# Optimization experiments

Hardware: AMD Instinct MI355X
Metric: run time of the kernel (lower is better)

The kernel has to match this reference:

```python
import jax, jax.numpy as jnp
import numpy as np

K = 7            # kernel size per spatial dim
HALF = K // 2    # 3
WIN = K * K      # 49


def _rel_dist():
    # matches torch: meshgrid('ij') of arange(k)-k//2, euclidean dist, flattened row-major
    c = np.arange(K, dtype=np.float32) - HALF
    gi, gj = np.meshgrid(c, c, indexing='ij')
    return jnp.asarray(np.sqrt(gi ** 2 + gj ** 2).reshape(-1))


def _unfold2d(t):
    B, H, W, C = t.shape
    p = jnp.pad(t, ((0, 0), (HALF, HALF), (HALF, HALF), (0, 0)))
    wins = [p[:, i:i + H, j:j + W, :] for i in range(K) for j in range(K)]
    return jnp.stack(wins, axis=3)


def setup_inputs() -> dict:
    key = jax.random.key(0)
    k1, k2, k3, k4, k5 = jax.random.split(key, 5)
    B, H, W, C = 4, 64, 64, 128
    x = jax.random.normal(k1, (B, H, W, C), dtype=jnp.float32)
    W_qkv = jax.random.normal(k2, (C, 3 * C), dtype=jnp.float32) * (C ** -0.5)
    # width_proj is zero-initialized in the module; use small random values to exercise the soft mask
    W_width = jax.random.normal(k3, (C, 1), dtype=jnp.float32) * 0.02
    b_width = jax.random.normal(k4, (1,), dtype=jnp.float32) * 0.02
    W_out = jax.random.normal(k5, (C, C), dtype=jnp.float32) * (C ** -0.5)
    return {"x": x, "W_qkv": W_qkv, "W_width": W_width, "b_width": b_width, "W_out": W_out}


def reference(x, W_qkv, W_width, b_width, W_out):
    B, H, W, C = x.shape
    L = H * W
    scale = C ** -0.5
    rel_dist = _rel_dist()
    max_dist = rel_dist.max()

    qkv = x @ W_qkv                              # (B,H,W,3C)
    q, k, v = jnp.split(qkv, 3, axis=-1)
    width = jax.nn.sigmoid(x @ W_width + b_width) * max_dist + 0.5  # (B,H,W,1)

    k_win = _unfold2d(k).reshape(B, L, WIN, C)
    v_win = _unfold2d(v).reshape(B, L, WIN, C)
    q_flat = q.reshape(B, L, C)
    width_flat = width.reshape(B, L, 1)

    scores = jnp.einsum('blc,blwc->blw', q_flat, k_win) * scale
    soft_mask = jax.nn.sigmoid((width_flat - rel_dist) * 5.0)
    scores = scores - (1.0 - soft_mask) * 10000.0
    attn = jax.nn.softmax(scores, axis=-1)
    out = jnp.einsum('blw,blwc->blc', attn, v_win).reshape(B, H, W, C)
    return (out + v) @ W_out
```

## Files before the change

### kernel.cpp

```cpp
#include <hip/hip_runtime.h>

#define C 128
#define NPIX 16384
#define THREE_C 384

typedef unsigned short u16;
typedef unsigned int u32;
typedef short bf16x8 __attribute__((ext_vector_type(8)));
typedef float f32x4 __attribute__((ext_vector_type(4)));

__device__ __forceinline__ float bf2f(u16 h) { return __uint_as_float(((u32)h) << 16); }
__device__ __forceinline__ u16 f2bf(float f) {
    u32 b = __float_as_uint(f);
    b += 0x7FFF + ((b >> 16) & 1);
    return (u16)(b >> 16);
}
__device__ __forceinline__ u32 pack2(float a, float b) {
    return (u32)f2bf(a) | ((u32)f2bf(b) << 16);
}

#define GST 136

__global__ __launch_bounds__(256) void qkv_kernel(const float* __restrict__ x,
                                                  const float* __restrict__ Wqkv,
                                                  const float* __restrict__ Wwidth,
                                                  const float* __restrict__ bwidth,
                                                  const float* __restrict__ Wout,
                                                  u16* __restrict__ qb,
                                                  u16* __restrict__ kb,
                                                  u16* __restrict__ vb,
                                                  float* __restrict__ width_g,
                                                  u16* __restrict__ wot) {
    __shared__ u16 xs[64 * GST];
    __shared__ u16 wt[128 * GST];
    const int task = ((int)(blockIdx.x & 7)) * 96 + ((int)blockIdx.x >> 3);
    const int rb = task / 3;
    const int nb = task % 3;
    const int p0 = rb * 64;
    const int tid = threadIdx.x;
    const int wv = tid >> 6;
    const int l = tid & 63;
    const int l15 = l & 15;
    const int l4 = l >> 4;

#pragma unroll
    for (int t = 0; t < 8; ++t) {
        const int f = tid + t * 256;
        const int kq = f & 31, r = f >> 5;
        const float4 xv = *(const float4*)(x + (size_t)(p0 + r) * C + kq * 4);
        uint2 pk;
        pk.x = pack2(xv.x, xv.y);
        pk.y = pack2(xv.z, xv.w);
        *(uint2*)&xs[r * GST + kq * 4] = pk;
    }
#pragma unroll
    for (int t = 0; t < 16; ++t) {
        const int f = tid + t * 256;
        const int c = f & 127, kq = f >> 7;
        const float w0 = Wqkv[(size_t)(kq * 4 + 0) * THREE_C + nb * 128 + c];
        const float w1 = Wqkv[(size_t)(kq * 4 + 1) * THREE_C + nb * 128 + c];
        const float w2 = Wqkv[(size_t)(kq * 4 + 2) * THREE_C + nb * 128 + c];
        const float w3 = Wqkv[(size_t)(kq * 4 + 3) * THREE_C + nb * 128 + c];
        uint2 pk;
        pk.x = pack2(w0, w1);
        pk.y = pack2(w2, w3);
        *(uint2*)&wt[c * GST + kq * 4] = pk;
    }
    if (task < 8) {
        const int base = (task * 256 + tid) * 8;
        const int c = base >> 7, k0 = base & 127;
        uint4 pk;
        pk.x = pack2(Wout[(size_t)(k0 + 0) * C + c], Wout[(size_t)(k0 + 1) * C + c]);
        pk.y = pack2(Wout[(size_t)(k0 + 2) * C + c], Wout[(size_t)(k0 + 3) * C + c]);
        pk.z = pack2(Wout[(size_t)(k0 + 4) * C + c], Wout[(size_t)(k0 + 5) * C + c]);
        pk.w = pack2(Wout[(size_t)(k0 + 6) * C + c], Wout[(size_t)(k0 + 7) * C + c]);
        *(uint4*)&wot[base] = pk;
    }
    __syncthreads();

    if (nb == 0 && tid < 64) {
        float wacc = 0.f;
#pragma unroll
        for (int kk = 0; kk < C; ++kk) wacc += bf2f(xs[tid * GST + kk]) * Wwidth[kk];
        const float z = wacc + bwidth[0];
        width_g[p0 + tid] = (1.f / (1.f + __expf(-z))) * 4.242640687f + 0.5f;
    }

    const int strip = wv * 16;
    bf16x8 af[4];
#pragma unroll
    for (int kf = 0; kf < 4; ++kf)
        af[kf] = *(const bf16x8*)&xs[(strip + l15) * GST + kf * 32 + l4 * 8];

    f32x4 acc[8];
#pragma unroll
    for (int nf = 0; nf < 8; ++nf) acc[nf] = (f32x4){0.f, 0.f, 0.f, 0.f};
#pragma unroll
    for (int nf = 0; nf < 8; ++nf) {
#pragma unroll
        for (int kf = 0; kf < 4; ++kf) {
            const bf16x8 bf = *(const bf16x8*)&wt[(nf * 16 + l15) * GST + kf * 32 + l4 * 8];
            acc[nf] = __builtin_amdgcn_mfma_f32_16x16x32_bf16(af[kf], bf, acc[nf], 0, 0, 0);
        }
    }

    u16* dst = (nb == 0) ? qb : (nb == 1) ? kb : vb;
#pragma unroll
    for (int nf = 0; nf < 8; ++nf) {
        const int col = nf * 16 + l15;
#pragma unroll
        for (int r = 0; r < 4; ++r) {
            const int row = strip + l4 * 4 + r;
            dst[(size_t)(p0 + row) * C + col] = f2bf(acc[nf][r]);
        }
    }
}

#define HSTRIDE 136
#define TSTRIDE 236
#define VSWZ(ch, h) ((h) ^ ((((ch) >> 3) & 3) << 3))

__global__ __launch_bounds__(1024) void attn_kernel(const u16* __restrict__ qb,
                                                    const u16* __restrict__ kb,
                                                    const u16* __restrict__ vb,
                                                    const float* __restrict__ width_g,
                                                    const u16* __restrict__ wot,
                                                    float* __restrict__ out) {
    __shared__ u16 Kl[208 * HSTRIDE];
    __shared__ u16 Vt[128 * TSTRIDE];
    __shared__ u16 Pl[64 * TSTRIDE];
    __shared__ float rsum[4][64];
    __shared__ float wdl[64];

    const int tid = threadIdx.x;
    const int wv = tid >> 6;
    const int l = tid & 63;
    const int l15 = l & 15;
    const int l4 = l >> 4;

    const int W = ((int)blockIdx.x & 7) * 32 + ((int)blockIdx.x >> 3);
    const int b = W >> 6;
    const int t = W & 63;
    const int i0 = (t >> 3) * 8;
    const int j0 = (t & 7) * 8;
    const int pbase = b * 4096;

    if (tid < 64)
        wdl[tid] = width_g[pbase + (i0 + (tid >> 3)) * 64 + j0 + (tid & 7)];

    const uint4 z4 = make_uint4(0, 0, 0, 0);
    uint4 kreg[4];
    int koff[4];
    bool kw[4];
#pragma unroll
    for (int rr = 0; rr < 4; ++rr) {
        const int f = tid + rr * 1024;
        kw[rr] = (f < 3328);
        kreg[rr] = z4;
        const int c = f & 15, h = f >> 4;
        koff[rr] = h * HSTRIDE + c * 8;
        if (kw[rr] && h < 196) {
            const int hi = (h * 2341) >> 15;
            const int hj = h - hi * 14;
            const int ii = i0 - 3 + hi, jj = j0 - 3 + hj;
            if (((unsigned)ii < 64u) && ((unsigned)jj < 64u))
                kreg[rr] = *(const uint4*)(kb + (size_t)(pbase + ii * 64 + jj) * C + c * 8);
        }
    }
    uint4 va[2], vz[2];
    int vc8[2], vh[2];
    bool vw[2];
#pragma unroll
    for (int rr = 0; rr < 2; ++rr) {
        const int f = tid + rr * 1024;
        vw[rr] = (f < 1792);
        va[rr] = z4; vz[rr] = z4;
        const int c8 = f & 15, h = ((f >> 4) * 2) & 255;
        vc8[rr] = c8; vh[rr] = h;
        if (vw[rr]) {
            {
                const int hi = (h * 2341) >> 15;
                const int hj = h - hi * 14;
                const int ii = i0 - 3 + hi, jj = j0 - 3 + hj;
                if ((h < 196) && ((unsigned)ii < 64u) && ((unsigned)jj < 64u))
                    va[rr] = *(const uint4*)(vb + (size_t)(pbase + ii * 64 + jj) * C + c8 * 8);
            }
            {
                const int h1 = h + 1;
                const int hi = (h1 * 2341) >> 15;
                const int hj = h1 - hi * 14;
                const int ii = i0 - 3 + hi, jj = j0 - 3 + hj;
                if ((h1 < 196) && ((unsigned)ii < 64u) && ((unsigned)jj < 64u))
                    vz[rr] = *(const uint4*)(vb + (size_t)(pbase + ii * 64 + jj) * C + c8 * 8);
            }
        }
    }
#pragma unroll
    for (int rr = 0; rr < 4; ++rr)
        if (kw[rr]) *(uint4*)&Kl[koff[rr]] = kreg[rr];
#pragma unroll
    for (int rr = 0; rr < 2; ++rr) {
        if (vw[rr]) {
            union { uint4 u4; u16 us[8]; } ua, uz;
            ua.u4 = va[rr]; uz.u4 = vz[rr];
            const int c8 = vc8[rr], h = vh[rr];
#pragma unroll
            for (int s = 0; s < 8; ++s) {
                const int ch = c8 * 8 + s;
                *(u32*)&Vt[ch * TSTRIDE + VSWZ(ch, h)] = (u32)ua.us[s] | ((u32)uz.us[s] << 16);
            }
        }
    }

    const int strip = wv >> 2;
    const int g = wv & 3;
    bf16x8 qf[4];
    {
        const int qr = strip * 16 + l15;
        const int p = pbase + (i0 + (qr >> 3)) * 64 + j0 + (qr & 7);
#pragma unroll
        for (int kf = 0; kf < 4; ++kf)
            qf[kf] = *(const bf16x8*)(qb + (size_t)p * C + kf * 32 + l4 * 8);
    }
    __syncthreads();

    f32x4 sv[4];
#pragma unroll
    for (int tt = 0; tt < 4; ++tt) {
        const int nf = g + 4 * tt;
        f32x4 acc = {0.f, 0.f, 0.f, 0.f};
        if (nf < 13) {
            const u16* kr = Kl + (nf * 16 + l15) * HSTRIDE + l4 * 8;
#pragma unroll
            for (int kf = 0; kf < 4; ++kf)
                acc = __builtin_amdgcn_mfma_f32_16x16x32_bf16(
                    qf[kf], *(const bf16x8*)(kr + kf * 32), acc, 0, 0, 0);
        }
        sv[tt] = acc;
    }

    uint4 wcopy0 = *(const uint4*)(wot + tid * 8);
    uint4 wcopy1 = *(const uint4*)(wot + (tid + 1024) * 8);

    const int qrb = strip * 16 + l4 * 4;
    float wdr[4];
#pragma unroll
    for (int r = 0; r < 4; ++r) wdr[r] = wdl[qrb + r];
    float smr[4] = {0.f, 0.f, 0.f, 0.f};
#pragma unroll
    for (int tt = 0; tt < 4; ++tt) {
        const int nf = g + 4 * tt;
        if (nf < 13) {
            const int n = nf * 16 + l15;
            const int hi = (n * 2341) >> 15;
            const int hj = n - hi * 14;
#pragma unroll
            for (int r = 0; r < 4; ++r) {
                const int qr = qrb + r;
                const int di = hi - 3 - (qr >> 3);
                const int dj = hj - 3 - (qr & 7);
                const bool valid = ((unsigned)(di + 3) <= 6u) && ((unsigned)(dj + 3) <= 6u);
                float e = 0.f;
                if (valid) {
                    const float rd = sqrtf((float)(di * di + dj * dj));
                    const float sm = 1.f / (1.f + __expf(-5.f * (wdr[r] - rd)));
                    e = __expf(sv[tt][r] * 0.08838834765f - (1.f - sm) * 10000.f);
                }
                sv[tt][r] = e;
                smr[r] += e;
                Pl[qr * TSTRIDE + n] = f2bf(e);
            }
        } else if (nf == 13) {
            const int n = 208 + l15;
#pragma unroll
            for (int r = 0; r < 4; ++r)
                Pl[(qrb + r) * TSTRIDE + n] = 0;
        }
    }
#pragma unroll
    for (int r = 0; r < 4; ++r) {
        float s = smr[r];
        s += __shfl_xor(s, 1);
        s += __shfl_xor(s, 2);
        s += __shfl_xor(s, 4);
        s += __shfl_xor(s, 8);
        smr[r] = s;
    }
    if (l15 == 0) {
#pragma unroll
        for (int r = 0; r < 4; ++r) rsum[g][qrb + r] = smr[r];
    }
    __syncthreads();

    u16* wtl = Kl;
    {
        const int c0 = tid >> 4, k0 = (tid & 15) * 8;
        *(uint4*)&wtl[c0 * GST + k0] = wcopy0;
        const int c1 = 64 + (tid >> 4);
        *(uint4*)&wtl[c1 * GST + k0] = wcopy1;
    }

    float invr[4];
#pragma unroll
    for (int r = 0; r < 4; ++r) {
        const int qr = qrb + r;
        invr[r] = 1.f / (rsum[0][qr] + rsum[1][qr] + rsum[2][qr] + rsum[3][qr]);
    }

    f32x4 oacc[2];
    oacc[0] = (f32x4){0.f, 0.f, 0.f, 0.f};
    oacc[1] = (f32x4){0.f, 0.f, 0.f, 0.f};
#pragma unroll
    for (int kf = 0; kf < 7; ++kf) {
        const bf16x8 pa = *(const bf16x8*)(Pl + (strip * 16 + l15) * TSTRIDE + kf * 32 + l4 * 8);
#pragma unroll
        for (int nf2 = 0; nf2 < 2; ++nf2) {
            const int ch = g * 32 + nf2 * 16 + l15;
            const bf16x8 vf = *(const bf16x8*)(Vt + ch * TSTRIDE + VSWZ(ch, kf * 32 + l4 * 8));
            oacc[nf2] = __builtin_amdgcn_mfma_f32_16x16x32_bf16(pa, vf, oacc[nf2], 0, 0, 0);
        }
    }

    u16* ylds = Kl + 128 * GST;
#pragma unroll
    for (int nf2 = 0; nf2 < 2; ++nf2) {
        const int cch = g * 32 + nf2 * 16 + l15;
#pragma unroll
        for (int r = 0; r < 4; ++r) {
            const int qr = qrb + r;
            const int h = 45 + (qr >> 3) * 14 + (qr & 7);
            const float vv = bf2f(Vt[cch * TSTRIDE + VSWZ(cch, h)]);
            ylds[qr * GST + cch] = f2bf(oacc[nf2][r] * invr[r] + vv);
        }
    }
    __syncthreads();

    bf16x8 yf[4];
#pragma unroll
    for (int kf = 0; kf < 4; ++kf)
        yf[kf] = *(const bf16x8*)&ylds[(strip * 16 + l15) * GST + kf * 32 + l4 * 8];

    f32x4 oc[2];
    oc[0] = (f32x4){0.f, 0.f, 0.f, 0.f};
    oc[1] = (f32x4){0.f, 0.f, 0.f, 0.f};
#pragma unroll
    for (int u = 0; u < 2; ++u) {
        const int nf = g + 4 * u;
#pragma unroll
        for (int kf = 0; kf < 4; ++kf) {
            const bf16x8 bf = *(const bf16x8*)&wtl[(nf * 16 + l15) * GST + kf * 32 + l4 * 8];
            oc[u] = __builtin_amdgcn_mfma_f32_16x16x32_bf16(yf[kf], bf, oc[u], 0, 0, 0);
        }
    }
#pragma unroll
    for (int u = 0; u < 2; ++u) {
        const int col = (g + 4 * u) * 16 + l15;
#pragma unroll
        for (int r = 0; r < 4; ++r) {
            const int qr = qrb + r;
            const int p = pbase + (i0 + (qr >> 3)) * 64 + j0 + (qr & 7);
            out[(size_t)p * C + col] = oc[u][r];
        }
    }
}

extern "C" void kernel_launch(void* const* d_in, const int* in_sizes, int n_in,
                              void* d_out, int out_size, void* d_ws, size_t ws_size,
                              hipStream_t stream) {
    const float* x      = (const float*)d_in[0];
    const float* Wqkv   = (const float*)d_in[1];
    const float* Wwidth = (const float*)d_in[2];
    const float* bwidth = (const float*)d_in[3];
    const float* Wout   = (const float*)d_in[4];
    float* out = (float*)d_out;

    u16* qb = (u16*)d_ws;
    u16* kb = qb + (size_t)NPIX * C;
    u16* vb = kb + (size_t)NPIX * C;
    float* width = (float*)(vb + (size_t)NPIX * C);
    u16* wot = (u16*)(width + NPIX);

    qkv_kernel<<<768, 256, 0, stream>>>(x, Wqkv, Wwidth, bwidth, Wout, qb, kb, vb, width, wot);
    attn_kernel<<<256, 1024, 0, stream>>>(qb, kb, vb, width, wot, out);
}
```

Measured before the change: 26.96 us.

## Fold Q and K projections into a precomputed Wk·Wqᵀ matrix

Q and K are no longer materialized. Scores are computed as x_q · M · x_kᵀ with M = Wk·Wqᵀ, which a small side job in the prep kernel computes. The prep kernel now only computes V, width and a bf16 copy of x, which roughly thirds its GEMM work and global writes. The attention kernel loads x windows instead of K and does an extra small 64x128x128 MFMA per tile. It also needs extra LDS, more barriers and an extra bf16 rounding of the intermediate x·M product.

```diff
diff --git a/kernel.cpp b/kernel.cpp
--- a/kernel.cpp
+++ b/kernel.cpp
@@ -21,97 +21,161 @@
 
 #define GST 136
 
-__global__ __launch_bounds__(256) void qkv_kernel(const float* __restrict__ x,
-                                                  const float* __restrict__ Wqkv,
-                                                  const float* __restrict__ Wwidth,
-                                                  const float* __restrict__ bwidth,
-                                                  const float* __restrict__ Wout,
-                                                  u16* __restrict__ qb,
-                                                  u16* __restrict__ kb,
-                                                  u16* __restrict__ vb,
-                                                  float* __restrict__ width_g,
-                                                  u16* __restrict__ wot) {
-    __shared__ u16 xs[64 * GST];
-    __shared__ u16 wt[128 * GST];
-    const int task = ((int)(blockIdx.x & 7)) * 96 + ((int)blockIdx.x >> 3);
-    const int rb = task / 3;
-    const int nb = task % 3;
-    const int p0 = rb * 64;
+__global__ __launch_bounds__(256) void vprep_kernel(const float* __restrict__ x,
+                                                    const float* __restrict__ Wqkv,
+                                                    const float* __restrict__ Wwidth,
+                                                    const float* __restrict__ bwidth,
+                                                    const float* __restrict__ Wout,
+                                                    u16* __restrict__ xbb,
+                                                    u16* __restrict__ vb,
+                                                    float* __restrict__ width_g,
+                                                    u16* __restrict__ wot,
+                                                    u16* __restrict__ mtw) {
+    __shared__ u16 SL[26112];
+    const int bid = blockIdx.x;
     const int tid = threadIdx.x;
     const int wv = tid >> 6;
     const int l = tid & 63;
     const int l15 = l & 15;
     const int l4 = l >> 4;
 
-#pragma unroll
-    for (int t = 0; t < 8; ++t) {
-        const int f = tid + t * 256;
-        const int kq = f & 31, r = f >> 5;
-        const float4 xv = *(const float4*)(x + (size_t)(p0 + r) * C + kq * 4);
-        uint2 pk;
-        pk.x = pack2(xv.x, xv.y);
-        pk.y = pack2(xv.z, xv.w);
-        *(uint2*)&xs[r * GST + kq * 4] = pk;
-    }
-#pragma unroll
-    for (int t = 0; t < 16; ++t) {
-        const int f = tid + t * 256;
-        const int c = f & 127, kq = f >> 7;
-        const float w0 = Wqkv[(size_t)(kq * 4 + 0) * THREE_C + nb * 128 + c];
-        const float w1 = Wqkv[(size_t)(kq * 4 + 1) * THREE_C + nb * 128 + c];
-        const float w2 = Wqkv[(size_t)(kq * 4 + 2) * THREE_C + nb * 128 + c];
-        const float w3 = Wqkv[(size_t)(kq * 4 + 3) * THREE_C + nb * 128 + c];
-        uint2 pk;
-        pk.x = pack2(w0, w1);
-        pk.y = pack2(w2, w3);
-        *(uint2*)&wt[c * GST + kq * 4] = pk;
-    }
-    if (task < 8) {
-        const int base = (task * 256 + tid) * 8;
-        const int c = base >> 7, k0 = base & 127;
-        uint4 pk;
-        pk.x = pack2(Wout[(size_t)(k0 + 0) * C + c], Wout[(size_t)(k0 + 1) * C + c]);
-        pk.y = pack2(Wout[(size_t)(k0 + 2) * C + c], Wout[(size_t)(k0 + 3) * C + c]);
-        pk.z = pack2(Wout[(size_t)(k0 + 4) * C + c], Wout[(size_t)(k0 + 5) * C + c]);
-        pk.w = pack2(Wout[(size_t)(k0 + 6) * C + c], Wout[(size_t)(k0 + 7) * C + c]);
-        *(uint4*)&wot[base] = pk;
-    }
-    __syncthreads();
-
-    if (nb == 0 && tid < 64) {
-        float wacc = 0.f;
-#pragma unroll
-        for (int kk = 0; kk < C; ++kk) wacc += bf2f(xs[tid * GST + kk]) * Wwidth[kk];
-        const float z = wacc + bwidth[0];
-        width_g[p0 + tid] = (1.f / (1.f + __expf(-z))) * 4.242640687f + 0.5f;
-    }
-
-    const int strip = wv * 16;
-    bf16x8 af[4];
-#pragma unroll
-    for (int kf = 0; kf < 4; ++kf)
-        af[kf] = *(const bf16x8*)&xs[(strip + l15) * GST + kf * 32 + l4 * 8];
-
-    f32x4 acc[8];
-#pragma unroll
-    for (int nf = 0; nf < 8; ++nf) acc[nf] = (f32x4){0.f, 0.f, 0.f, 0.f};
-#pragma unroll
-    for (int nf = 0; nf < 8; ++nf) {
-#pragma unroll
-        for (int kf = 0; kf < 4; ++kf) {
-            const bf16x8 bf = *(const bf16x8*)&wt[(nf * 16 + l15) * GST + kf * 32 + l4 * 8];
-            acc[nf] = __builtin_amdgcn_mfma_f32_16x16x32_bf16(af[kf], bf, acc[nf], 0, 0, 0);
-        }
-    }
-
-    u16* dst = (nb == 0) ? qb : (nb == 1) ? kb : vb;
-#pragma unroll
-    for (int nf = 0; nf < 8; ++nf) {
-        const int col = nf * 16 + l15;
-#pragma unroll
-        for (int r = 0; r < 4; ++r) {
-            const int row = strip + l4 * 4 + r;
-            dst[(size_t)(p0 + row) * C + col] = f2bf(acc[nf][r]);
+    if (bid < 512) {
+        u16* xs = SL;
+        u16* wt = SL + 32 * GST;
+        const int task = ((bid & 7) << 6) + (bid >> 3);
+        const int p0 = task * 32;
+
+#pragma unroll
+        for (int t = 0; t < 4; ++t) {
+            const int f = tid + t * 256;
+            const int kq = f & 31, r = f >> 5;
+            const float4 xv = *(const float4*)(x + (size_t)(p0 + r) * C + kq * 4);
+            uint2 pk;
+            pk.x = pack2(xv.x, xv.y);
+            pk.y = pack2(xv.z, xv.w);
+            *(uint2*)&xs[r * GST + kq * 4] = pk;
+        }
+#pragma unroll
+        for (int t = 0; t < 16; ++t) {
+            const int f = tid + t * 256;
+            const int c = f & 127, kq = f >> 7;
+            const float w0 = Wqkv[(size_t)(kq * 4 + 0) * THREE_C + 256 + c];
+            const float w1 = Wqkv[(size_t)(kq * 4 + 1) * THREE_C + 256 + c];
+            const float w2 = Wqkv[(size_t)(kq * 4 + 2) * THREE_C + 256 + c];
+            const float w3 = Wqkv[(size_t)(kq * 4 + 3) * THREE_C + 256 + c];
+            uint2 pk;
+            pk.x = pack2(w0, w1);
+            pk.y = pack2(w2, w3);
+            *(uint2*)&wt[c * GST + kq * 4] = pk;
+        }
+        __syncthreads();
+
+        if (tid < 32) {
+            float wacc = 0.f;
+#pragma unroll
+            for (int kk = 0; kk < C; ++kk) wacc += bf2f(xs[tid * GST + kk]) * Wwidth[kk];
+            const float z = wacc + bwidth[0];
+            width_g[p0 + tid] = (1.f / (1.f + __expf(-z))) * 4.242640687f + 0.5f;
+        }
+
+#pragma unroll
+        for (int i = 0; i < 2; ++i) {
+            const int id = tid + 256 * i;
+            const int r = id >> 4, c16 = id & 15;
+            *(uint4*)(xbb + (size_t)(p0 + r) * C + c16 * 8) = *(const uint4*)&xs[r * GST + c16 * 8];
+        }
+
+        const int strip = (wv & 1) * 16;
+        const int nh = wv >> 1;
+        bf16x8 af[4];
+#pragma unroll
+        for (int kf = 0; kf < 4; ++kf)
+            af[kf] = *(const bf16x8*)&xs[(strip + l15) * GST + kf * 32 + l4 * 8];
+        f32x4 acc[4];
+#pragma unroll
+        for (int i = 0; i < 4; ++i) acc[i] = (f32x4){0.f, 0.f, 0.f, 0.f};
+#pragma unroll
+        for (int nfi = 0; nfi < 4; ++nfi) {
+            const int nf = nh * 4 + nfi;
+#pragma unroll
+            for (int kf = 0; kf < 4; ++kf) {
+                const bf16x8 bf = *(const bf16x8*)&wt[(nf * 16 + l15) * GST + kf * 32 + l4 * 8];
+                acc[nfi] = __builtin_amdgcn_mfma_f32_16x16x32_bf16(af[kf], bf, acc[nfi], 0, 0, 0);
+            }
+        }
+#pragma unroll
+        for (int nfi = 0; nfi < 4; ++nfi) {
+            const int col = (nh * 4 + nfi) * 16 + l15;
+#pragma unroll
+            for (int r = 0; r < 4; ++r) {
+                const int row = strip + l4 * 4 + r;
+                vb[(size_t)(p0 + row) * C + col] = f2bf(acc[nfi][r]);
+            }
+        }
+    } else {
+        u16* wkl = SL;
+        u16* wql = SL + 64 * GST;
+        const int blk = bid - 512;
+        const int d0 = blk * 64;
+
+#pragma unroll
+        for (int t = 0; t < 8; ++t) {
+            const int f = tid + t * 256;
+            const int kq = f & 31, r = f >> 5;
+            const float4 wv4 = *(const float4*)(Wqkv + (size_t)(d0 + r) * THREE_C + 128 + kq * 4);
+            uint2 pk;
+            pk.x = pack2(wv4.x, wv4.y);
+            pk.y = pack2(wv4.z, wv4.w);
+            *(uint2*)&wkl[r * GST + kq * 4] = pk;
+        }
+#pragma unroll
+        for (int t = 0; t < 16; ++t) {
+            const int f = tid + t * 256;
+            const int kq = f & 31, r = f >> 7 == 0 ? (f >> 5) : (f >> 5);
+            const int rr = f >> 5;
+            const float4 wv4 = *(const float4*)(Wqkv + (size_t)rr * THREE_C + kq * 4);
+            uint2 pk;
+            pk.x = pack2(wv4.x, wv4.y);
+            pk.y = pack2(wv4.z, wv4.w);
+            *(uint2*)&wql[rr * GST + kq * 4] = pk;
+        }
+#pragma unroll
+        for (int it = 0; it < 4; ++it) {
+            const int u4i = blk * 1024 + tid + 256 * it;
+            const int base = u4i * 8;
+            const int c = base >> 7, k0 = base & 127;
+            uint4 pk;
+            pk.x = pack2(Wout[(size_t)(k0 + 0) * C + c], Wout[(size_t)(k0 + 1) * C + c]);
+            pk.y = pack2(Wout[(size_t)(k0 + 2) * C + c], Wout[(size_t)(k0 + 3) * C + c]);
+            pk.z = pack2(Wout[(size_t)(k0 + 4) * C + c], Wout[(size_t)(k0 + 5) * C + c]);
+            pk.w = pack2(Wout[(size_t)(k0 + 6) * C + c], Wout[(size_t)(k0 + 7) * C + c]);
+            *(uint4*)&wot[base] = pk;
+        }
+        __syncthreads();
+
+        bf16x8 af[4];
+#pragma unroll
+        for (int kf = 0; kf < 4; ++kf)
+            af[kf] = *(const bf16x8*)&wkl[(wv * 16 + l15) * GST + kf * 32 + l4 * 8];
+        f32x4 acc[8];
+#pragma unroll
+        for (int nf = 0; nf < 8; ++nf) acc[nf] = (f32x4){0.f, 0.f, 0.f, 0.f};
+#pragma unroll
+        for (int nf = 0; nf < 8; ++nf) {
+#pragma unroll
+            for (int kf = 0; kf < 4; ++kf) {
+                const bf16x8 bf = *(const bf16x8*)&wql[(nf * 16 + l15) * GST + kf * 32 + l4 * 8];
+                acc[nf] = __builtin_amdgcn_mfma_f32_16x16x32_bf16(af[kf], bf, acc[nf], 0, 0, 0);
+            }
+        }
+#pragma unroll
+        for (int nf = 0; nf < 8; ++nf) {
+            const int c = nf * 16 + l15;
+#pragma unroll
+            for (int r = 0; r < 4; ++r) {
+                const int d = d0 + wv * 16 + l4 * 4 + r;
+                mtw[(size_t)d * C + c] = f2bf(acc[nf][r]);
+            }
         }
     }
 }
@@ -120,17 +184,18 @@
 #define TSTRIDE 236
 #define VSWZ(ch, h) ((h) ^ ((((ch) >> 3) & 3) << 3))
 
-__global__ __launch_bounds__(1024) void attn_kernel(const u16* __restrict__ qb,
-                                                    const u16* __restrict__ kb,
+__global__ __launch_bounds__(1024) void attn_kernel(const u16* __restrict__ xbb,
                                                     const u16* __restrict__ vb,
                                                     const float* __restrict__ width_g,
                                                     const u16* __restrict__ wot,
+                                                    const u16* __restrict__ mtw,
                                                     float* __restrict__ out) {
-    __shared__ u16 Kl[208 * HSTRIDE];
-    __shared__ u16 Vt[128 * TSTRIDE];
-    __shared__ u16 Pl[64 * TSTRIDE];
+    __shared__ u16 SL[75904];
     __shared__ float rsum[4][64];
     __shared__ float wdl[64];
+    u16* Xl = SL;
+    u16* MT = SL + 208 * HSTRIDE;
+    u16* Vt = MT + 128 * GST;
 
     const int tid = threadIdx.x;
     const int wv = tid >> 6;
@@ -164,7 +229,7 @@
             const int hj = h - hi * 14;
             const int ii = i0 - 3 + hi, jj = j0 - 3 + hj;
             if (((unsigned)ii < 64u) && ((unsigned)jj < 64u))
-                kreg[rr] = *(const uint4*)(kb + (size_t)(pbase + ii * 64 + jj) * C + c * 8);
+                kreg[rr] = *(const uint4*)(xbb + (size_t)(pbase + ii * 64 + jj) * C + c * 8);
         }
     }
     uint4 va[2], vz[2];
@@ -195,9 +260,18 @@
             }
         }
     }
+    uint4 mcp[2];
+    int moff[2];
+#pragma unroll
+    for (int i = 0; i < 2; ++i) {
+        const int id = tid + 1024 * i;
+        const int d = id >> 4, c8 = id & 15;
+        mcp[i] = *(const uint4*)(mtw + (size_t)d * C + c8 * 8);
+        moff[i] = d * GST + c8 * 8;
+    }
 #pragma unroll
     for (int rr = 0; rr < 4; ++rr)
-        if (kw[rr]) *(uint4*)&Kl[koff[rr]] = kreg[rr];
+        if (kw[rr]) *(uint4*)&Xl[koff[rr]] = kreg[rr];
 #pragma unroll
     for (int rr = 0; rr < 2; ++rr) {
         if (vw[rr]) {
@@ -211,30 +285,61 @@
             }
         }
     }
+#pragma unroll
+    for (int i = 0; i < 2; ++i) *(uint4*)&MT[moff[i]] = mcp[i];
+    __syncthreads();
 
     const int strip = wv >> 2;
     const int g = wv & 3;
-    bf16x8 qf[4];
+    bf16x8 xf[4];
     {
         const int qr = strip * 16 + l15;
-        const int p = pbase + (i0 + (qr >> 3)) * 64 + j0 + (qr & 7);
+        const int hown = 45 + (qr >> 3) * 14 + (qr & 7);
 #pragma unroll
         for (int kf = 0; kf < 4; ++kf)
-            qf[kf] = *(const bf16x8*)(qb + (size_t)p * C + kf * 32 + l4 * 8);
-    }
-    __syncthreads();
-
+            xf[kf] = *(const bf16x8*)&Xl[hown * HSTRIDE + kf * 32 + l4 * 8];
+    }
+    f32x4 tacc[2];
+    tacc[0] = (f32x4){0.f, 0.f, 0.f, 0.f};
+    tacc[1] = (f32x4){0.f, 0.f, 0.f, 0.f};
+#pragma unroll
+    for (int u = 0; u < 2; ++u) {
+        const int nf = g + 4 * u;
+#pragma unroll
+        for (int kf = 0; kf < 4; ++kf) {
+            const bf16x8 bf = *(const bf16x8*)&MT[(nf * 16 + l15) * GST + kf * 32 + l4 * 8];
+            tacc[u] = __builtin_amdgcn_mfma_f32_16x16x32_bf16(xf[kf], bf, tacc[u], 0, 0, 0);
+        }
+    }
+    __syncthreads();
+
+    u16* TD = MT;
+#pragma unroll
+    for (int u = 0; u < 2; ++u) {
+        const int col = (g + 4 * u) * 16 + l15;
+#pragma unroll
+        for (int r = 0; r < 4; ++r) {
+            const int row = strip * 16 + l4 * 4 + r;
+            TD[row * GST + col] = f2bf(tacc[u][r]);
+        }
+    }
+    __syncthreads();
+
+    bf16x8 tf[4];
+#pragma unroll
+    for (int kf = 0; kf < 4; ++kf)
+        tf[kf] = *(const bf16x8*)&TD[(strip * 16 + l15) * GST + kf * 32 + l4 * 8];
     f32x4 sv[4];
 #pragma unroll
     for (int tt = 0; tt < 4; ++tt) {
         const int nf = g + 4 * tt;
         f32x4 acc = {0.f, 0.f, 0.f, 0.f};
         if (nf < 13) {
-            const u16* kr = Kl + (nf * 16 + l15) * HSTRIDE + l4 * 8;
+            const u16* xr = Xl + (nf * 16 + l15) * HSTRIDE + l4 * 8;
 #pragma unroll
             for (int kf = 0; kf < 4; ++kf)
                 acc = __builtin_amdgcn_mfma_f32_16x16x32_bf16(
-                    qf[kf], *(const bf16x8*)(kr + kf * 32), acc, 0, 0, 0);
+                    tf[kf], *(const bf16x8*)(xr + kf * 32), acc, 0, 0, 0);
         }
         sv[tt] = acc;
     }
@@ -268,13 +373,7 @@
                 }
                 sv[tt][r] = e;
                 smr[r] += e;
-                Pl[qr * TSTRIDE + n] = f2bf(e);
-            }
-        } else if (nf == 13) {
-            const int n = 208 + l15;
-#pragma unroll
-            for (int r = 0; r < 4; ++r)
-                Pl[(qrb + r) * TSTRIDE + n] = 0;
+            }
         }
     }
 #pragma unroll
@@ -292,27 +391,43 @@
     }
     __syncthreads();
 
-    u16* wtl = Kl;
+    u16* Pb = Xl;
+    u16* YL = Xl + 64 * TSTRIDE;
+    u16* WO = MT;
+#pragma unroll
+    for (int tt = 0; tt < 4; ++tt) {
+        const int nf = g + 4 * tt;
+        if (nf < 13) {
+            const int n = nf * 16 + l15;
+#pragma unroll
+            for (int r = 0; r < 4; ++r)
+                Pb[(qrb + r) * TSTRIDE + n] = f2bf(sv[tt][r]);
+        } else if (nf == 13) {
+            const int n = 208 + l15;
+#pragma unroll
+            for (int r = 0; r < 4; ++r)
+                Pb[(qrb + r) * TSTRIDE + n] = 0;
+        }
+    }
     {
         const int c0 = tid >> 4, k0 = (tid & 15) * 8;
-        *(uint4*)&wtl[c0 * GST + k0] = wcopy0;
-        const int c1 = 64 + (tid >> 4);
-        *(uint4*)&wtl[c1 * GST + k0] = wcopy1;
-    }
-
+        *(uint4*)&WO[c0 * GST + k0] = wcopy0;
+        *(uint4*)&WO[(64 + c0) * GST + k0] = wcopy1;
+    }
     float invr[4];
 #pragma unroll
     for (int r = 0; r < 4; ++r) {
         const int qr = qrb + r;
         invr[r] = 1.f / (rsum[0][qr] + rsum[1][qr] + rsum[2][qr] + rsum[3][qr]);
     }
+    __syncthreads();
 
     f32x4 oacc[2];
     oacc[0] = (f32x4){0.f, 0.f, 0.f, 0.f};
     oacc[1] = (f32x4){0.f, 0.f, 0.f, 0.f};
 #pragma unroll
     for (int kf = 0; kf < 7; ++kf) {
-        const bf16x8 pa = *(const bf16x8*)(Pl + (strip * 16 + l15) * TSTRIDE + kf * 32 + l4 * 8);
+        const bf16x8 pa = *(const bf16x8*)(Pb + (strip * 16 + l15) * TSTRIDE + kf * 32 + l4 * 8);
 #pragma unroll
         for (int nf2 = 0; nf2 < 2; ++nf2) {
             const int ch = g * 32 + nf2 * 16 + l15;
@@ -320,8 +435,6 @@
             oacc[nf2] = __builtin_amdgcn_mfma_f32_16x16x32_bf16(pa, vf, oacc[nf2], 0, 0, 0);
         }
     }
-
-    u16* ylds = Kl + 128 * GST;
 #pragma unroll
     for (int nf2 = 0; nf2 < 2; ++nf2) {
         const int cch = g * 32 + nf2 * 16 + l15;
@@ -330,7 +443,7 @@
             const int qr = qrb + r;
             const int h = 45 + (qr >> 3) * 14 + (qr & 7);
             const float vv = bf2f(Vt[cch * TSTRIDE + VSWZ(cch, h)]);
-            ylds[qr * GST + cch] = f2bf(oacc[nf2][r] * invr[r] + vv);
+            YL[qr * GST + cch] = f2bf(oacc[nf2][r] * invr[r] + vv);
         }
     }
     __syncthreads();
@@ -338,8 +451,7 @@
     bf16x8 yf[4];
 #pragma unroll
     for (int kf = 0; kf < 4; ++kf)
-        yf[kf] = *(const bf16x8*)&ylds[(strip * 16 + l15) * GST + kf * 32 + l4 * 8];
-
+        yf[kf] = *(const bf16x8*)&YL[(strip * 16 + l15) * GST + kf * 32 + l4 * 8];
     f32x4 oc[2];
     oc[0] = (f32x4){0.f, 0.f, 0.f, 0.f};
     oc[1] = (f32x4){0.f, 0.f, 0.f, 0.f};
@@ -348,7 +460,7 @@
         const int nf = g + 4 * u;
 #pragma unroll
         for (int kf = 0; kf < 4; ++kf) {
-            const bf16x8 bf = *(const bf16x8*)&wtl[(nf * 16 + l15) * GST + kf * 32 + l4 * 8];
+            const bf16x8 bf = *(const bf16x8*)&WO[(nf * 16 + l15) * GST + kf * 32 + l4 * 8];
             oc[u] = __builtin_amdgcn_mfma_f32_16x16x32_bf16(yf[kf], bf, oc[u], 0, 0, 0);
         }
     }
@@ -374,12 +486,12 @@
     const float* Wout   = (const float*)d_in[4];
     float* out = (float*)d_out;
 
-    u16* qb = (u16*)d_ws;
-    u16* kb = qb + (size_t)NPIX * C;
-    u16* vb = kb + (size_t)NPIX * C;
+    u16* xbb = (u16*)d_ws;
+    u16* vb  = xbb + (size_t)NPIX * C;
     float* width = (float*)(vb + (size_t)NPIX * C);
     u16* wot = (u16*)(width + NPIX);
-
-    qkv_kernel<<<768, 256, 0, stream>>>(x, Wqkv, Wwidth, bwidth, Wout, qb, kb, vb, width, wot);
-    attn_kernel<<<256, 1024, 0, stream>>>(qb, kb, vb, width, wot, out);
+    u16* mtw = wot + 128 * 128;
+
+    vprep_kernel<<<514, 256, 0, stream>>>(x, Wqkv, Wwidth, bwidth, Wout, xbb, vb, width, wot, mtw);
+    attn_kernel<<<256, 1024, 0, stream>>>(xbb, vb, width, wot, mtw, out);
 }
```

New measurement: 36.86 us. +36.7%, slower.

## Shrink attention tile to 4x4 pixels with 1024 blocks of 512 threads

Applied to the files above, without the earlier changes.

The attention kernel now handles a 4x4 query tile with a 10x10 halo instead of an 8x8 tile with a 14x14 halo. It launches 1024 blocks of 512 threads with launch bounds allowing four blocks per CU, and loads W_out fragments straight from global memory into registers instead of staging them in LDS. The aim is more blocks and better occupancy on the 256-CU device, where 256 large blocks underfill it. The cost is more redundant K/V halo loading per output pixel (100 vs 196 halo rows for 16 vs 64 queries), and the V swizzle is dropped, so LDS bank conflicts may appear.

```diff
diff --git a/kernel.cpp b/kernel.cpp
--- a/kernel.cpp
+++ b/kernel.cpp
@@ -116,21 +116,19 @@
     }
 }
 
-#define HSTRIDE 136
-#define TSTRIDE 236
-#define VSWZ(ch, h) ((h) ^ ((((ch) >> 3) & 3) << 3))
-
-__global__ __launch_bounds__(1024) void attn_kernel(const u16* __restrict__ qb,
-                                                    const u16* __restrict__ kb,
-                                                    const u16* __restrict__ vb,
-                                                    const float* __restrict__ width_g,
-                                                    const u16* __restrict__ wot,
-                                                    float* __restrict__ out) {
-    __shared__ u16 Kl[208 * HSTRIDE];
-    __shared__ u16 Vt[128 * TSTRIDE];
-    __shared__ u16 Pl[64 * TSTRIDE];
-    __shared__ float rsum[4][64];
-    __shared__ float wdl[64];
+#define HST 136
+
+__global__ __launch_bounds__(512, 4) void attn_kernel(const u16* __restrict__ qb,
+                                                      const u16* __restrict__ kb,
+                                                      const u16* __restrict__ vb,
+                                                      const float* __restrict__ width_g,
+                                                      const u16* __restrict__ wot,
+                                                      float* __restrict__ out) {
+    __shared__ u16 Kl[112 * HST];
+    __shared__ u16 Vt[128 * HST];
+    __shared__ u16 Pl[16 * HST];
+    __shared__ float rsum[7][16];
+    __shared__ float wdl[16];
 
     const int tid = threadIdx.x;
     const int wv = tid >> 6;
@@ -138,15 +136,15 @@
     const int l15 = l & 15;
     const int l4 = l >> 4;
 
-    const int W = ((int)blockIdx.x & 7) * 32 + ((int)blockIdx.x >> 3);
-    const int b = W >> 6;
-    const int t = W & 63;
-    const int i0 = (t >> 3) * 8;
-    const int j0 = (t & 7) * 8;
+    const int W = ((int)(blockIdx.x & 7) << 7) + ((int)blockIdx.x >> 3);
+    const int b = W >> 8;
+    const int t = W & 255;
+    const int i0 = (t >> 4) * 4;
+    const int j0 = (t & 15) * 4;
     const int pbase = b * 4096;
 
-    if (tid < 64)
-        wdl[tid] = width_g[pbase + (i0 + (tid >> 3)) * 64 + j0 + (tid & 7)];
+    if (tid < 16)
+        wdl[tid] = width_g[pbase + (i0 + (tid >> 2)) * 64 + j0 + (tid & 3)];
 
     const uint4 z4 = make_uint4(0, 0, 0, 0);
     uint4 kreg[4];
@@ -154,14 +152,14 @@
     bool kw[4];
 #pragma unroll
     for (int rr = 0; rr < 4; ++rr) {
-        const int f = tid + rr * 1024;
-        kw[rr] = (f < 3328);
+        const int f = tid + rr * 512;
+        kw[rr] = (f < 1792);
         kreg[rr] = z4;
         const int c = f & 15, h = f >> 4;
-        koff[rr] = h * HSTRIDE + c * 8;
-        if (kw[rr] && h < 196) {
-            const int hi = (h * 2341) >> 15;
-            const int hj = h - hi * 14;
+        koff[rr] = h * HST + c * 8;
+        if (kw[rr] && h < 100) {
+            const int hi = (h * 3277) >> 15;
+            const int hj = h - hi * 10;
             const int ii = i0 - 3 + hi, jj = j0 - 3 + hj;
             if (((unsigned)ii < 64u) && ((unsigned)jj < 64u))
                 kreg[rr] = *(const uint4*)(kb + (size_t)(pbase + ii * 64 + jj) * C + c * 8);
@@ -172,28 +170,36 @@
     bool vw[2];
 #pragma unroll
     for (int rr = 0; rr < 2; ++rr) {
-        const int f = tid + rr * 1024;
-        vw[rr] = (f < 1792);
+        const int f = tid + rr * 512;
+        vw[rr] = (f < 896);
         va[rr] = z4; vz[rr] = z4;
-        const int c8 = f & 15, h = ((f >> 4) * 2) & 255;
+        const int c8 = f & 15, h = ((f >> 4) * 2) & 127;
         vc8[rr] = c8; vh[rr] = h;
         if (vw[rr]) {
             {
-                const int hi = (h * 2341) >> 15;
-                const int hj = h - hi * 14;
+                const int hi = (h * 3277) >> 15;
+                const int hj = h - hi * 10;
                 const int ii = i0 - 3 + hi, jj = j0 - 3 + hj;
-                if ((h < 196) && ((unsigned)ii < 64u) && ((unsigned)jj < 64u))
+                if ((h < 100) && ((unsigned)ii < 64u) && ((unsigned)jj < 64u))
                     va[rr] = *(const uint4*)(vb + (size_t)(pbase + ii * 64 + jj) * C + c8 * 8);
             }
             {
                 const int h1 = h + 1;
-                const int hi = (h1 * 2341) >> 15;
-                const int hj = h1 - hi * 14;
+                const int hi = (h1 * 3277) >> 15;
+                const int hj = h1 - hi * 10;
                 const int ii = i0 - 3 + hi, jj = j0 - 3 + hj;
-                if ((h1 < 196) && ((unsigned)ii < 64u) && ((unsigned)jj < 64u))
+                if ((h1 < 100) && ((unsigned)ii < 64u) && ((unsigned)jj < 64u))
                     vz[rr] = *(const uint4*)(vb + (size_t)(pbase + ii * 64 + jj) * C + c8 * 8);
             }
         }
+    }
+    bf16x8 qf[4];
+    {
+        const int qr = l15;
+        const int p = pbase + (i0 + (qr >> 2)) * 64 + j0 + (qr & 3);
+#pragma unroll
+        for (int kf = 0; kf < 4; ++kf)
+            qf[kf] = *(const bf16x8*)(qb + (size_t)p * C + kf * 32 + l4 * 8);
     }
 #pragma unroll
     for (int rr = 0; rr < 4; ++rr)
@@ -207,159 +213,120 @@
 #pragma unroll
             for (int s = 0; s < 8; ++s) {
                 const int ch = c8 * 8 + s;
-                *(u32*)&Vt[ch * TSTRIDE + VSWZ(ch, h)] = (u32)ua.us[s] | ((u32)uz.us[s] << 16);
+                *(u32*)&Vt[ch * HST + h] = (u32)ua.us[s] | ((u32)uz.us[s] << 16);
             }
         }
     }
-
-    const int strip = wv >> 2;
-    const int g = wv & 3;
-    bf16x8 qf[4];
     {
-        const int qr = strip * 16 + l15;
-        const int p = pbase + (i0 + (qr >> 3)) * 64 + j0 + (qr & 7);
+        const int f = tid + 512;
+        if (f >= 896) {
+            const int ch = f - 896;
+#pragma unroll
+            for (int s = 0; s < 8; ++s)
+                *(u32*)&Vt[ch * HST + 112 + s * 2] = 0u;
+        }
+    }
+    __syncthreads();
+
+    const int g = wv;
+    f32x4 sv = {0.f, 0.f, 0.f, 0.f};
+    if (g < 7) {
+        const u16* kr = Kl + (g * 16 + l15) * HST + l4 * 8;
 #pragma unroll
         for (int kf = 0; kf < 4; ++kf)
-            qf[kf] = *(const bf16x8*)(qb + (size_t)p * C + kf * 32 + l4 * 8);
-    }
-    __syncthreads();
-
-    f32x4 sv[4];
-#pragma unroll
-    for (int tt = 0; tt < 4; ++tt) {
-        const int nf = g + 4 * tt;
-        f32x4 acc = {0.f, 0.f, 0.f, 0.f};
-        if (nf < 13) {
-            const u16* kr = Kl + (nf * 16 + l15) * HSTRIDE + l4 * 8;
-#pragma unroll
-            for (int kf = 0; kf < 4; ++kf)
-                acc = __builtin_amdgcn_mfma_f32_16x16x32_bf16(
-                    qf[kf], *(const bf16x8*)(kr + kf * 32), acc, 0, 0, 0);
-        }
-        sv[tt] = acc;
-    }
-
-    uint4 wcopy0 = *(const uint4*)(wot + tid * 8);
-    uint4 wcopy1 = *(const uint4*)(wot + (tid + 1024) * 8);
-
-    const int qrb = strip * 16 + l4 * 4;
+            sv = __builtin_amdgcn_mfma_f32_16x16x32_bf16(
+                qf[kf], *(const bf16x8*)(kr + kf * 32), sv, 0, 0, 0);
+    }
+
+    bf16x8 wof[4];
+#pragma unroll
+    for (int kf = 0; kf < 4; ++kf)
+        wof[kf] = *(const bf16x8*)(wot + (size_t)(g * 16 + l15) * 128 + kf * 32 + l4 * 8);
+
+    const int qrb = l4 * 4;
     float wdr[4];
 #pragma unroll
     for (int r = 0; r < 4; ++r) wdr[r] = wdl[qrb + r];
-    float smr[4] = {0.f, 0.f, 0.f, 0.f};
-#pragma unroll
-    for (int tt = 0; tt < 4; ++tt) {
-        const int nf = g + 4 * tt;
-        if (nf < 13) {
-            const int n = nf * 16 + l15;
-            const int hi = (n * 2341) >> 15;
-            const int hj = n - hi * 14;
-#pragma unroll
-            for (int r = 0; r < 4; ++r) {
-                const int qr = qrb + r;
-                const int di = hi - 3 - (qr >> 3);
-                const int dj = hj - 3 - (qr & 7);
-                const bool valid = ((unsigned)(di + 3) <= 6u) && ((unsigned)(dj + 3) <= 6u);
-                float e = 0.f;
-                if (valid) {
+    if (g < 7) {
+        const int n = g * 16 + l15;
+        float smr[4];
+        int hi = 0, hj = 0;
+        const bool ncol = (n < 100);
+        if (ncol) { hi = (n * 3277) >> 15; hj = n - hi * 10; }
+#pragma unroll
+        for (int r = 0; r < 4; ++r) {
+            const int row = qrb + r;
+            float e = 0.f;
+            if (ncol) {
+                const int di = hi - 3 - (row >> 2);
+                const int dj = hj - 3 - (row & 3);
+                if (((unsigned)(di + 3) <= 6u) && ((unsigned)(dj + 3) <= 6u)) {
                     const float rd = sqrtf((float)(di * di + dj * dj));
                     const float sm = 1.f / (1.f + __expf(-5.f * (wdr[r] - rd)));
-                    e = __expf(sv[tt][r] * 0.08838834765f - (1.f - sm) * 10000.f);
+                    e = __expf(sv[r] * 0.08838834765f - (1.f - sm) * 10000.f);
                 }
-                sv[tt][r] = e;
-                smr[r] += e;
-                Pl[qr * TSTRIDE + n] = f2bf(e);
             }
-        } else if (nf == 13) {
-            const int n = 208 + l15;
-#pragma unroll
-            for (int r = 0; r < 4; ++r)
-                Pl[(qrb + r) * TSTRIDE + n] = 0;
-        }
-    }
+            smr[r] = e;
+            Pl[row * HST + n] = f2bf(e);
+        }
+#pragma unroll
+        for (int r = 0; r < 4; ++r) {
+            float s = smr[r];
+            s += __shfl_xor(s, 1);
+            s += __shfl_xor(s, 2);
+            s += __shfl_xor(s, 4);
+            s += __shfl_xor(s, 8);
+            if (l15 == 0) rsum[g][qrb + r] = s;
+        }
+    } else {
+#pragma unroll
+        for (int r = 0; r < 4; ++r)
+            Pl[(qrb + r) * HST + 112 + l15] = 0;
+    }
+    __syncthreads();
+
+    float invr[4];
 #pragma unroll
     for (int r = 0; r < 4; ++r) {
-        float s = smr[r];
-        s += __shfl_xor(s, 1);
-        s += __shfl_xor(s, 2);
-        s += __shfl_xor(s, 4);
-        s += __shfl_xor(s, 8);
-        smr[r] = s;
-    }
-    if (l15 == 0) {
-#pragma unroll
-        for (int r = 0; r < 4; ++r) rsum[g][qrb + r] = smr[r];
+        const int row = qrb + r;
+        invr[r] = 1.f / (rsum[0][row] + rsum[1][row] + rsum[2][row] + rsum[3][row]
+                       + rsum[4][row] + rsum[5][row] + rsum[6][row]);
+    }
+
+    f32x4 oacc = {0.f, 0.f, 0.f, 0.f};
+#pragma unroll
+    for (int kf = 0; kf < 4; ++kf) {
+        const bf16x8 pa = *(const bf16x8*)(Pl + l15 * HST + kf * 32 + l4 * 8);
+        const bf16x8 vf = *(const bf16x8*)(Vt + (g * 16 + l15) * HST + kf * 32 + l4 * 8);
+        oacc = __builtin_amdgcn_mfma_f32_16x16x32_bf16(pa, vf, oacc, 0, 0, 0);
+    }
+
+    u16* YL = Kl;
+    {
+        const int ch = g * 16 + l15;
+#pragma unroll
+        for (int r = 0; r < 4; ++r) {
+            const int row = qrb + r;
+            const int hown = 33 + (row >> 2) * 10 + (row & 3);
+            const float vv = bf2f(Vt[ch * HST + hown]);
+            YL[row * HST + ch] = f2bf(oacc[r] * invr[r] + vv);
+        }
     }
     __syncthreads();
 
-    u16* wtl = Kl;
+    f32x4 oc = {0.f, 0.f, 0.f, 0.f};
+#pragma unroll
+    for (int kf = 0; kf < 4; ++kf) {
+        const bf16x8 yf = *(const bf16x8*)(YL + l15 * HST + kf * 32 + l4 * 8);
+        oc = __builtin_amdgcn_mfma_f32_16x16x32_bf16(yf, wof[kf], oc, 0, 0, 0);
+    }
     {
-        const int c0 = tid >> 4, k0 = (tid & 15) * 8;
-        *(uint4*)&wtl[c0 * GST + k0] = wcopy0;
-        const int c1 = 64 + (tid >> 4);
-        *(uint4*)&wtl[c1 * GST + k0] = wcopy1;
-    }
-
-    float invr[4];
-#pragma unroll
-    for (int r = 0; r < 4; ++r) {
-        const int qr = qrb + r;
-        invr[r] = 1.f / (rsum[0][qr] + rsum[1][qr] + rsum[2][qr] + rsum[3][qr]);
-    }
-
-    f32x4 oacc[2];
-    oacc[0] = (f32x4){0.f, 0.f, 0.f, 0.f};
-    oacc[1] = (f32x4){0.f, 0.f, 0.f, 0.f};
-#pragma unroll
-    for (int kf = 0; kf < 7; ++kf) {
-        const bf16x8 pa = *(const bf16x8*)(Pl + (strip * 16 + l15) * TSTRIDE + kf * 32 + l4 * 8);
-#pragma unroll
-        for (int nf2 = 0; nf2 < 2; ++nf2) {
-            const int ch = g * 32 + nf2 * 16 + l15;
-            const bf16x8 vf = *(const bf16x8*)(Vt + ch * TSTRIDE + VSWZ(ch, kf * 32 + l4 * 8));
-            oacc[nf2] = __builtin_amdgcn_mfma_f32_16x16x32_bf16(pa, vf, oacc[nf2], 0, 0, 0);
-        }
-    }
-
-    u16* ylds = Kl + 128 * GST;
-#pragma unroll
-    for (int nf2 = 0; nf2 < 2; ++nf2) {
-        const int cch = g * 32 + nf2 * 16 + l15;
-#pragma unroll
-        for (int r = 0; r < 4; ++r) {
-            const int qr = qrb + r;
-            const int h = 45 + (qr >> 3) * 14 + (qr & 7);
-            const float vv = bf2f(Vt[cch * TSTRIDE + VSWZ(cch, h)]);
-            ylds[qr * GST + cch] = f2bf(oacc[nf2][r] * invr[r] + vv);
-        }
-    }
-    __syncthreads();
-
-    bf16x8 yf[4];
-#pragma unroll
-    for (int kf = 0; kf < 4; ++kf)
-        yf[kf] = *(const bf16x8*)&ylds[(strip * 16 + l15) * GST + kf * 32 + l4 * 8];
-
-    f32x4 oc[2];
-    oc[0] = (f32x4){0.f, 0.f, 0.f, 0.f};
-    oc[1] = (f32x4){0.f, 0.f, 0.f, 0.f};
-#pragma unroll
-    for (int u = 0; u < 2; ++u) {
-        const int nf = g + 4 * u;
-#pragma unroll
-        for (int kf = 0; kf < 4; ++kf) {
-            const bf16x8 bf = *(const bf16x8*)&wtl[(nf * 16 + l15) * GST + kf * 32 + l4 * 8];
-            oc[u] = __builtin_amdgcn_mfma_f32_16x16x32_bf16(yf[kf], bf, oc[u], 0, 0, 0);
-        }
-    }
-#pragma unroll
-    for (int u = 0; u < 2; ++u) {
-        const int col = (g + 4 * u) * 16 + l15;
-#pragma unroll
-        for (int r = 0; r < 4; ++r) {
-            const int qr = qrb + r;
-            const int p = pbase + (i0 + (qr >> 3)) * 64 + j0 + (qr & 7);
-            out[(size_t)p * C + col] = oc[u][r];
+        const int col = g * 16 + l15;
+#pragma unroll
+        for (int r = 0; r < 4; ++r) {
+            const int row = qrb + r;
+            const int p = pbase + (i0 + (row >> 2)) * 64 + j0 + (row & 3);
+            out[(size_t)p * C + col] = oc[r];
         }
     }
 }
@@ -381,5 +348,5 @@
     u16* wot = (u16*)(width + NPIX);
 
     qkv_kernel<<<768, 256, 0, stream>>>(x, Wqkv, Wwidth, bwidth, Wout, qb, kb, vb, width, wot);
-    attn_kernel<<<256, 1024, 0, stream>>>(qb, kb, vb, width, wot, out);
-}
+    attn_kernel<<<1024, 512, 0, stream>>>(qb, kb, vb, width, wot, out);
+}
```

After: 32.01 us. +18.7%, slower.
